# Kernel tuning notes

Hardware: AMD Instinct MI355X
Metric: run time of the kernel (lower is better)

Reference implementation:

```python
import jax, jax.numpy as jnp
import numpy as np

N_NODES = 100000
N_EDGES = 3200000
IN_FEATS = 128
OUT_FEATS = 16
NEG_SLOPE = 0.2


def setup_inputs() -> dict:
    key = jax.random.key(0)
    k1, k2, k3, k4, k5, k6 = jax.random.split(key, 6)
    h = jax.random.normal(k1, (N_NODES, IN_FEATS), dtype=jnp.float32)
    src = jax.random.randint(k2, (N_EDGES,), 0, N_NODES, dtype=jnp.int64)
    dst = jax.random.randint(k3, (N_EDGES,), 0, N_NODES, dtype=jnp.int64)
    W = jax.random.normal(k4, (OUT_FEATS, IN_FEATS), dtype=jnp.float32) * (1.0 / np.sqrt(IN_FEATS))
    a_l = jax.random.normal(k5, (1, OUT_FEATS), dtype=jnp.float32) * (1.0 / np.sqrt(OUT_FEATS))
    a_r = jax.random.normal(k6, (1, OUT_FEATS), dtype=jnp.float32) * (1.0 / np.sqrt(OUT_FEATS))
    return {"h": h, "src": src, "dst": dst, "W": W, "a_l": a_l, "a_r": a_r}


def reference(h, src, dst, W, a_l, a_r):
    N = h.shape[0]
    # node projection: h @ fc.weight.T  -> [N, out]
    hW = h @ W.T
    # per-node attention logits: [N, 1]
    el = hW @ a_l.T
    er = hW @ a_r.T
    # u_add_v: per-edge logit e = el[src] + er[dst], then leaky_relu(0.2)
    e = jax.nn.leaky_relu(el[src] + er[dst], negative_slope=NEG_SLOPE)  # [E, 1]
    # edge_softmax over edges grouped by destination node (numerically stable)
    emax = jax.ops.segment_max(e, dst, num_segments=N)  # [N, 1], -inf for empty
    emax = jnp.where(jnp.isfinite(emax), emax, 0.0)
    e_exp = jnp.exp(e - emax[dst])
    esum = jax.ops.segment_sum(e_exp, dst, num_segments=N)  # [N, 1]
    alpha = e_exp / jnp.maximum(esum[dst], 1e-16)  # [E, 1]
    # u_mul_e + sum: weighted aggregation of source features at destinations
    out = jax.ops.segment_sum(hW[src] * alpha, dst, num_segments=N)  # [N, out]
    return out
```

## Files before the change

### kernel.cpp

```cpp
#include <hip/hip_runtime.h>
#include <hip/hip_bf16.h>
#include <stdint.h>

#define IN_F 128
#define OUT_F 16
#define NEG_SLOPE 0.2f
#define LB_BITS 7
#define LB_NODES 128
#define NB 782
#define CAP 4608
#define SC_E 8192

#define SMEM_BYTES (12512 + 1024 + SC_E * 4)

__device__ __forceinline__ float u2f(uint32_t u) {
  union { uint32_t i; float f; } c;
  c.i = u;
  return c.f;
}

__global__ __launch_bounds__(256) void proj_scatter_kernel(
    const float* __restrict__ h, const float* __restrict__ W,
    const float* __restrict__ a_l, const float* __restrict__ a_r,
    const int* __restrict__ src, const int* __restrict__ dst,
    __hip_bfloat16* __restrict__ hWbf, float* __restrict__ el,
    float* __restrict__ er, int* __restrict__ cursor,
    uint32_t* __restrict__ payload, int N, int E, int scatBlocks) {
  __shared__ __align__(16) uint8_t smem[SMEM_BYTES];
  int t = threadIdx.x;

  if ((int)blockIdx.x < scatBlocks) {
    int* hist = (int*)smem;
    int* pref = hist + NB;
    int* gbase = pref + NB;
    int* rank = gbase + NB;
    int* tsum = rank + NB;
    uint32_t* sortedP = (uint32_t*)(tsum + 256);

    int start = blockIdx.x * SC_E;
    int end = min(E, start + SC_E);
    int cnt = end - start;

    for (int i = t; i < NB; i += 256) { hist[i] = 0; rank[i] = 0; }
    __syncthreads();

    const int4* d4 = (const int4*)(dst + start);
    int n4 = cnt >> 2;
    for (int i = t; i < n4; i += 256) {
      int4 d = d4[i];
      atomicAdd(&hist[d.x >> LB_BITS], 1);
      atomicAdd(&hist[d.y >> LB_BITS], 1);
      atomicAdd(&hist[d.z >> LB_BITS], 1);
      atomicAdd(&hist[d.w >> LB_BITS], 1);
    }
    for (int i = start + (n4 << 2) + t; i < end; i += 256)
      atomicAdd(&hist[dst[i] >> LB_BITS], 1);
    __syncthreads();

    {
      int b0 = t * 4;
      int s_loc = 0;
      if (b0 < NB) {
        int lim = min(b0 + 4, NB);
        for (int j = b0; j < lim; ++j) s_loc += hist[j];
      }
      tsum[t] = s_loc;
    }
    __syncthreads();
    {
      int pre = 0;
      for (int j = 0; j < t; ++j) pre += tsum[j];
      int b0 = t * 4;
      if (b0 < NB) {
        int lim = min(b0 + 4, NB);
        int run = pre;
        for (int j = b0; j < lim; ++j) {
          pref[j] = run;
          int c = hist[j];
          run += c;
          gbase[j] = c ? atomicAdd(&cursor[j * 16], c) : 0;
        }
      }
    }
    __syncthreads();

    const int4* s4 = (const int4*)(src + start);
    for (int i = t; i < n4; i += 256) {
      int4 d = d4[i];
      int4 s = s4[i];
#pragma unroll
      for (int j = 0; j < 4; ++j) {
        int dd = j == 0 ? d.x : j == 1 ? d.y : j == 2 ? d.z : d.w;
        int ss = j == 0 ? s.x : j == 1 ? s.y : j == 2 ? s.z : s.w;
        int b = dd >> LB_BITS;
        int r = atomicAdd(&rank[b], 1);
        sortedP[pref[b] + r] =
            ((uint32_t)ss << LB_BITS) | (uint32_t)(dd & (LB_NODES - 1));
      }
    }
    for (int i = start + (n4 << 2) + t; i < end; i += 256) {
      int dd = dst[i];
      int b = dd >> LB_BITS;
      int r = atomicAdd(&rank[b], 1);
      sortedP[pref[b] + r] =
          ((uint32_t)src[i] << LB_BITS) | (uint32_t)(dd & (LB_NODES - 1));
    }
    __syncthreads();

    int g16 = t >> 4, l16 = t & 15;
    for (int b = g16; b < NB; b += 16) {
      int c = hist[b];
      if (c == 0) continue;
      int p0 = pref[b];
      int gb = gbase[b];
      size_t g0 = (size_t)b * CAP + (size_t)gb;
      for (int j = l16; j < c; j += 16)
        if (gb + j < CAP) payload[g0 + j] = sortedP[p0 + j];
    }
  } else {
    float* Ws = (float*)smem;
    for (int i = t; i < OUT_F * IN_F; i += 256) Ws[i] = W[i];
    __syncthreads();

    int node = ((int)blockIdx.x - scatBlocks) * 256 + t;
    if (node >= N) return;

    const float4* hrow = (const float4*)(h + (size_t)node * IN_F);
    float acc[OUT_F];
#pragma unroll
    for (int f = 0; f < OUT_F; ++f) acc[f] = 0.f;

#pragma unroll 4
    for (int k = 0; k < IN_F / 4; ++k) {
      float4 hv = hrow[k];
#pragma unroll
      for (int f = 0; f < OUT_F; ++f) {
        float4 wv = ((const float4*)(Ws + f * IN_F))[k];
        acc[f] += hv.x * wv.x + hv.y * wv.y + hv.z * wv.z + hv.w * wv.w;
      }
    }

    union {
      unsigned short us[OUT_F];
      uint4 q[2];
    } pk;
#pragma unroll
    for (int f = 0; f < OUT_F; ++f) {
      __hip_bfloat16 b = __float2bfloat16(acc[f]);
      pk.us[f] = *reinterpret_cast<unsigned short*>(&b);
    }
    uint4* dstq = (uint4*)(hWbf + (size_t)node * OUT_F);
    dstq[0] = pk.q[0];
    dstq[1] = pk.q[1];

    float vl = 0.f, vr = 0.f;
#pragma unroll
    for (int f = 0; f < OUT_F; ++f) {
      vl += acc[f] * a_l[f];
      vr += acc[f] * a_r[f];
    }
    el[node] = vl;
    er[node] = vr;
  }
}

__global__ __launch_bounds__(512) void agg_kernel(
    const uint32_t* __restrict__ payload, const int* __restrict__ cursor,
    const __hip_bfloat16* __restrict__ hWbf, const float* __restrict__ el,
    const float* __restrict__ er, float* __restrict__ out, int N) {
  __shared__ __align__(16) uint32_t sorted[CAP];
  __shared__ __align__(16) float exS[CAP];
  __shared__ int hist[LB_NODES];
  __shared__ int pref[LB_NODES];
  __shared__ int rank[LB_NODES];
  uint32_t* kept = (uint32_t*)exS;

  int t = threadIdx.x;
  int b = blockIdx.x;
  size_t base = (size_t)b * CAP;
  int cnt = min(cursor[b * 16], CAP);
  int node0 = b << LB_BITS;

  if (t < LB_NODES) { hist[t] = 0; rank[t] = 0; }
  __syncthreads();

  const uint4* pay4 = (const uint4*)(payload + base);
  uint4* kept4 = (uint4*)kept;
  int n4 = (cnt + 3) >> 2;
  for (int i = t; i < n4; i += 512) {
    uint4 v = pay4[i];
    kept4[i] = v;
    int i0 = i << 2;
    if (i0 + 0 < cnt) atomicAdd(&hist[v.x & (LB_NODES - 1)], 1);
    if (i0 + 1 < cnt) atomicAdd(&hist[v.y & (LB_NODES - 1)], 1);
    if (i0 + 2 < cnt) atomicAdd(&hist[v.z & (LB_NODES - 1)], 1);
    if (i0 + 3 < cnt) atomicAdd(&hist[v.w & (LB_NODES - 1)], 1);
  }
  __syncthreads();

  if (t < LB_NODES) {
    int s = 0;
    for (int j = 0; j < t; ++j) s += hist[j];
    pref[t] = s;
  }
  __syncthreads();

  for (int i = t; i < cnt; i += 512) {
    uint32_t p = kept[i];
    int dl = (int)(p & (LB_NODES - 1));
    int r = atomicAdd(&rank[dl], 1);
    sorted[pref[dl] + r] = p;
  }
  __syncthreads();

  for (int i = t; i < cnt; i += 512) {
    uint32_t p = sorted[i];
    float x = el[p >> LB_BITS] + er[node0 + (int)(p & (LB_NODES - 1))];
    x = x > 0.f ? x : NEG_SLOPE * x;
    exS[i] = __expf(x);
  }
  __syncthreads();

  int g = t >> 2, f4 = t & 3;
  int node = node0 + g;
  if (node < N) {
    int k = pref[g];
    int kend = k + hist[g];
    float a0 = 0.f, a1 = 0.f, a2 = 0.f, a3 = 0.f, es = 0.f;
    const uint2* hw2 = (const uint2*)hWbf;
#pragma unroll 4
    for (; k < kend; ++k) {
      uint32_t p = sorted[k];
      float ex = exS[k];
      uint2 w = hw2[(size_t)(p >> LB_BITS) * 4 + f4];
      a0 += ex * u2f(w.x << 16);
      a1 += ex * u2f(w.x & 0xffff0000u);
      a2 += ex * u2f(w.y << 16);
      a3 += ex * u2f(w.y & 0xffff0000u);
      es += ex;
    }
    float inv = 1.0f / fmaxf(es, 1e-16f);
    float4 o = make_float4(a0 * inv, a1 * inv, a2 * inv, a3 * inv);
    ((float4*)(out + (size_t)node * OUT_F))[f4] = o;
  }
}

extern "C" void kernel_launch(void* const* d_in, const int* in_sizes, int n_in,
                              void* d_out, int out_size, void* d_ws, size_t ws_size,
                              hipStream_t stream) {
  const float* h   = (const float*)d_in[0];
  const int*   src = (const int*)d_in[1];
  const int*   dst = (const int*)d_in[2];
  const float* W   = (const float*)d_in[3];
  const float* a_l = (const float*)d_in[4];
  const float* a_r = (const float*)d_in[5];
  float* out = (float*)d_out;

  const int N = in_sizes[0] / IN_F;
  const int E = in_sizes[1];
  const int scatBlocks = (E + SC_E - 1) / SC_E;
  const int projBlocks = (N + 255) / 256;

  __hip_bfloat16* hWbf = (__hip_bfloat16*)d_ws;
  float* el = (float*)(hWbf + (size_t)N * OUT_F);
  float* er = el + N;
  int* cursor = (int*)(er + N);
  uint32_t* payload = (uint32_t*)(cursor + (size_t)NB * 16);

  hipMemsetAsync(cursor, 0, (size_t)NB * 16 * sizeof(int), stream);

  proj_scatter_kernel<<<scatBlocks + projBlocks, 256, 0, stream>>>(
      h, W, a_l, a_r, src, dst, hWbf, el, er, cursor, payload, N, E, scatBlocks);

  agg_kernel<<<NB, 512, 0, stream>>>(payload, cursor, hWbf, el, er, out, N);
}
```

Before: 180.9 us.

## Widen proj/scatter blocks, two nodes per projection thread, fuse agg exp pass

The fused projection/scatter kernel now runs 512-thread blocks. The scatter path reuses the histogram as the rank counter and derives bucket counts from a prefix array with a sentinel entry, which saves shared memory. Each projection thread computes two node rows so every shared W load serves two rows. In the aggregation kernel the payload staging copy is removed: the counting-sort pass rereads payload from global memory, computes the exponentiated logit inline using er values cached in shared memory, and drops one pass and one barrier. The risks are higher register pressure from the dual accumulators and a second global read of the payload.

```diff
diff --git a/kernel.cpp b/kernel.cpp
--- a/kernel.cpp
+++ b/kernel.cpp
@@ -10,8 +10,9 @@
 #define NB 782
 #define CAP 4608
 #define SC_E 8192
-
-#define SMEM_BYTES (12512 + 1024 + SC_E * 4)
+#define PROJ_M 2
+
+#define SMEM_BYTES (11436 + SC_E * 4)
 
 __device__ __forceinline__ float u2f(uint32_t u) {
   union { uint32_t i; float f; } c;
@@ -19,7 +20,7 @@
   return c.f;
 }
 
-__global__ __launch_bounds__(256) void proj_scatter_kernel(
+__global__ __launch_bounds__(512, 6) void proj_scatter_kernel(
     const float* __restrict__ h, const float* __restrict__ W,
     const float* __restrict__ a_l, const float* __restrict__ a_r,
     const int* __restrict__ src, const int* __restrict__ dst,
@@ -32,36 +33,35 @@
   if ((int)blockIdx.x < scatBlocks) {
     int* hist = (int*)smem;
     int* pref = hist + NB;
-    int* gbase = pref + NB;
-    int* rank = gbase + NB;
-    int* tsum = rank + NB;
-    uint32_t* sortedP = (uint32_t*)(tsum + 256);
+    int* gbase = pref + NB + 1;
+    int* tsum = gbase + NB;
+    uint32_t* sortedP = (uint32_t*)(tsum + 512);
 
     int start = blockIdx.x * SC_E;
     int end = min(E, start + SC_E);
     int cnt = end - start;
 
-    for (int i = t; i < NB; i += 256) { hist[i] = 0; rank[i] = 0; }
+    for (int i = t; i < NB; i += 512) hist[i] = 0;
     __syncthreads();
 
     const int4* d4 = (const int4*)(dst + start);
     int n4 = cnt >> 2;
-    for (int i = t; i < n4; i += 256) {
+    for (int i = t; i < n4; i += 512) {
       int4 d = d4[i];
       atomicAdd(&hist[d.x >> LB_BITS], 1);
       atomicAdd(&hist[d.y >> LB_BITS], 1);
       atomicAdd(&hist[d.z >> LB_BITS], 1);
       atomicAdd(&hist[d.w >> LB_BITS], 1);
     }
-    for (int i = start + (n4 << 2) + t; i < end; i += 256)
+    for (int i = start + (n4 << 2) + t; i < end; i += 512)
       atomicAdd(&hist[dst[i] >> LB_BITS], 1);
     __syncthreads();
 
     {
-      int b0 = t * 4;
+      int b0 = t * 2;
       int s_loc = 0;
       if (b0 < NB) {
-        int lim = min(b0 + 4, NB);
+        int lim = min(b0 + 2, NB);
         for (int j = b0; j < lim; ++j) s_loc += hist[j];
       }
       tsum[t] = s_loc;
@@ -70,22 +70,24 @@
     {
       int pre = 0;
       for (int j = 0; j < t; ++j) pre += tsum[j];
-      int b0 = t * 4;
+      int b0 = t * 2;
       if (b0 < NB) {
-        int lim = min(b0 + 4, NB);
+        int lim = min(b0 + 2, NB);
         int run = pre;
         for (int j = b0; j < lim; ++j) {
           pref[j] = run;
           int c = hist[j];
           run += c;
           gbase[j] = c ? atomicAdd(&cursor[j * 16], c) : 0;
+          hist[j] = 0;
         }
+        if (lim == NB) pref[NB] = run;
       }
     }
     __syncthreads();
 
     const int4* s4 = (const int4*)(src + start);
-    for (int i = t; i < n4; i += 256) {
+    for (int i = t; i < n4; i += 512) {
       int4 d = d4[i];
       int4 s = s4[i];
 #pragma unroll
@@ -93,25 +95,25 @@
         int dd = j == 0 ? d.x : j == 1 ? d.y : j == 2 ? d.z : d.w;
         int ss = j == 0 ? s.x : j == 1 ? s.y : j == 2 ? s.z : s.w;
         int b = dd >> LB_BITS;
-        int r = atomicAdd(&rank[b], 1);
+        int r = atomicAdd(&hist[b], 1);
         sortedP[pref[b] + r] =
             ((uint32_t)ss << LB_BITS) | (uint32_t)(dd & (LB_NODES - 1));
       }
     }
-    for (int i = start + (n4 << 2) + t; i < end; i += 256) {
+    for (int i = start + (n4 << 2) + t; i < end; i += 512) {
       int dd = dst[i];
       int b = dd >> LB_BITS;
-      int r = atomicAdd(&rank[b], 1);
+      int r = atomicAdd(&hist[b], 1);
       sortedP[pref[b] + r] =
           ((uint32_t)src[i] << LB_BITS) | (uint32_t)(dd & (LB_NODES - 1));
     }
     __syncthreads();
 
     int g16 = t >> 4, l16 = t & 15;
-    for (int b = g16; b < NB; b += 16) {
-      int c = hist[b];
+    for (int b = g16; b < NB; b += 32) {
+      int p0 = pref[b];
+      int c = pref[b + 1] - p0;
       if (c == 0) continue;
-      int p0 = pref[b];
       int gb = gbase[b];
       size_t g0 = (size_t)b * CAP + (size_t)gb;
       for (int j = l16; j < c; j += 16)
@@ -119,24 +121,30 @@
     }
   } else {
     float* Ws = (float*)smem;
-    for (int i = t; i < OUT_F * IN_F; i += 256) Ws[i] = W[i];
-    __syncthreads();
-
-    int node = ((int)blockIdx.x - scatBlocks) * 256 + t;
-    if (node >= N) return;
-
-    const float4* hrow = (const float4*)(h + (size_t)node * IN_F);
-    float acc[OUT_F];
-#pragma unroll
-    for (int f = 0; f < OUT_F; ++f) acc[f] = 0.f;
-
-#pragma unroll 4
+    for (int i = t; i < OUT_F * IN_F; i += 512) Ws[i] = W[i];
+    __syncthreads();
+
+    int blk = (int)blockIdx.x - scatBlocks;
+    int n0 = blk * (512 * PROJ_M) + t;
+    int n1 = n0 + 512;
+    bool v1 = n1 < N;
+    if (n0 >= N) return;
+
+    const float4* r0 = (const float4*)(h + (size_t)n0 * IN_F);
+    const float4* r1 = (const float4*)(h + (size_t)(v1 ? n1 : n0) * IN_F);
+
+    float acc0[OUT_F], acc1[OUT_F];
+#pragma unroll
+    for (int f = 0; f < OUT_F; ++f) { acc0[f] = 0.f; acc1[f] = 0.f; }
+
     for (int k = 0; k < IN_F / 4; ++k) {
-      float4 hv = hrow[k];
+      float4 h0 = r0[k];
+      float4 h1 = r1[k];
 #pragma unroll
       for (int f = 0; f < OUT_F; ++f) {
         float4 wv = ((const float4*)(Ws + f * IN_F))[k];
-        acc[f] += hv.x * wv.x + hv.y * wv.y + hv.z * wv.z + hv.w * wv.w;
+        acc0[f] += h0.x * wv.x + h0.y * wv.y + h0.z * wv.z + h0.w * wv.w;
+        acc1[f] += h1.x * wv.x + h1.y * wv.y + h1.z * wv.z + h1.w * wv.w;
       }
     }
 
@@ -146,21 +154,40 @@
     } pk;
 #pragma unroll
     for (int f = 0; f < OUT_F; ++f) {
-      __hip_bfloat16 b = __float2bfloat16(acc[f]);
+      __hip_bfloat16 b = __float2bfloat16(acc0[f]);
       pk.us[f] = *reinterpret_cast<unsigned short*>(&b);
     }
-    uint4* dstq = (uint4*)(hWbf + (size_t)node * OUT_F);
-    dstq[0] = pk.q[0];
-    dstq[1] = pk.q[1];
+    uint4* dq0 = (uint4*)(hWbf + (size_t)n0 * OUT_F);
+    dq0[0] = pk.q[0];
+    dq0[1] = pk.q[1];
 
     float vl = 0.f, vr = 0.f;
 #pragma unroll
     for (int f = 0; f < OUT_F; ++f) {
-      vl += acc[f] * a_l[f];
-      vr += acc[f] * a_r[f];
-    }
-    el[node] = vl;
-    er[node] = vr;
+      vl += acc0[f] * a_l[f];
+      vr += acc0[f] * a_r[f];
+    }
+    el[n0] = vl;
+    er[n0] = vr;
+
+    if (v1) {
+#pragma unroll
+      for (int f = 0; f < OUT_F; ++f) {
+        __hip_bfloat16 b = __float2bfloat16(acc1[f]);
+        pk.us[f] = *reinterpret_cast<unsigned short*>(&b);
+      }
+      uint4* dq1 = (uint4*)(hWbf + (size_t)n1 * OUT_F);
+      dq1[0] = pk.q[0];
+      dq1[1] = pk.q[1];
+      float wl = 0.f, wr = 0.f;
+#pragma unroll
+      for (int f = 0; f < OUT_F; ++f) {
+        wl += acc1[f] * a_l[f];
+        wr += acc1[f] * a_r[f];
+      }
+      el[n1] = wl;
+      er[n1] = wr;
+    }
   }
 }
 
@@ -173,7 +200,7 @@
   __shared__ int hist[LB_NODES];
   __shared__ int pref[LB_NODES];
   __shared__ int rank[LB_NODES];
-  uint32_t* kept = (uint32_t*)exS;
+  __shared__ float erS[LB_NODES];
 
   int t = threadIdx.x;
   int b = blockIdx.x;
@@ -181,15 +208,18 @@
   int cnt = min(cursor[b * 16], CAP);
   int node0 = b << LB_BITS;
 
-  if (t < LB_NODES) { hist[t] = 0; rank[t] = 0; }
+  if (t < LB_NODES) {
+    hist[t] = 0;
+    rank[t] = 0;
+    int nd = node0 + t;
+    erS[t] = nd < N ? er[nd] : 0.f;
+  }
   __syncthreads();
 
   const uint4* pay4 = (const uint4*)(payload + base);
-  uint4* kept4 = (uint4*)kept;
   int n4 = (cnt + 3) >> 2;
   for (int i = t; i < n4; i += 512) {
     uint4 v = pay4[i];
-    kept4[i] = v;
     int i0 = i << 2;
     if (i0 + 0 < cnt) atomicAdd(&hist[v.x & (LB_NODES - 1)], 1);
     if (i0 + 1 < cnt) atomicAdd(&hist[v.y & (LB_NODES - 1)], 1);
@@ -206,18 +236,14 @@
   __syncthreads();
 
   for (int i = t; i < cnt; i += 512) {
-    uint32_t p = kept[i];
+    uint32_t p = payload[base + i];
     int dl = (int)(p & (LB_NODES - 1));
     int r = atomicAdd(&rank[dl], 1);
-    sorted[pref[dl] + r] = p;
-  }
-  __syncthreads();
-
-  for (int i = t; i < cnt; i += 512) {
-    uint32_t p = sorted[i];
-    float x = el[p >> LB_BITS] + er[node0 + (int)(p & (LB_NODES - 1))];
+    int pos = pref[dl] + r;
+    sorted[pos] = p;
+    float x = el[p >> LB_BITS] + erS[dl];
     x = x > 0.f ? x : NEG_SLOPE * x;
-    exS[i] = __expf(x);
+    exS[pos] = __expf(x);
   }
   __syncthreads();
 
@@ -259,7 +285,7 @@
   const int N = in_sizes[0] / IN_F;
   const int E = in_sizes[1];
   const int scatBlocks = (E + SC_E - 1) / SC_E;
-  const int projBlocks = (N + 255) / 256;
+  const int projBlocks = (N + 512 * PROJ_M - 1) / (512 * PROJ_M);
 
   __hip_bfloat16* hWbf = (__hip_bfloat16*)d_ws;
   float* el = (float*)(hWbf + (size_t)N * OUT_F);
@@ -269,7 +295,7 @@
 
   hipMemsetAsync(cursor, 0, (size_t)NB * 16 * sizeof(int), stream);
 
-  proj_scatter_kernel<<<scatBlocks + projBlocks, 256, 0, stream>>>(
+  proj_scatter_kernel<<<scatBlocks + projBlocks, 512, 0, stream>>>(
       h, W, a_l, a_r, src, dst, hWbf, el, er, cursor, payload, N, E, scatBlocks);
 
   agg_kernel<<<NB, 512, 0, stream>>>(payload, cursor, hWbf, el, er, out, N);
```

Result: slower. 195.0 us (+7.8%).

## Fuse memset, scatter/projection and aggregation into one cooperative kernel

Applied to the files above, without the earlier changes.

Replaces the memset plus two kernel launches with a single cooperative kernel that zeroes the cursors, runs scatter and projection, then aggregation, separated by grid-wide syncs. The aim is to remove launch gaps and tail effects between stages. It also shrinks shared memory with 16-bit prefix arrays, switches to a wave-shuffle scan, fuses the sort and exp passes in aggregation, caches er in shared memory, and uses 256 threads with 8 features per thread. Grid sync only works if all ~1175 blocks fit co-resident; the cooperative launch may fail, in which case it falls back to separate launches.

```diff
diff --git a/kernel.cpp b/kernel.cpp
--- a/kernel.cpp
+++ b/kernel.cpp
@@ -1,6 +1,9 @@
 #include <hip/hip_runtime.h>
 #include <hip/hip_bf16.h>
+#include <hip/hip_cooperative_groups.h>
 #include <stdint.h>
+
+namespace cg = cooperative_groups;
 
 #define IN_F 128
 #define OUT_F 16
@@ -11,7 +14,20 @@
 #define CAP 4608
 #define SC_E 8192
 
-#define SMEM_BYTES (12512 + 1024 + SC_E * 4)
+#define OFF_HIST 0
+#define OFF_WSUM 3136
+#define OFF_PREF 3152
+#define OFF_GBASE 4720
+#define OFF_SORTP 6400
+#define SMEM_FUSED 39168
+
+#define AOFF_SORTED 0
+#define AOFF_EXS 18432
+#define AOFF_HIST 36864
+#define AOFF_PREF 37376
+#define AOFF_RANK 37888
+#define AOFF_ERS 38400
+#define SMEM_AGG 38912
 
 __device__ __forceinline__ float u2f(uint32_t u) {
   union { uint32_t i; float f; } c;
@@ -19,247 +35,329 @@
   return c.f;
 }
 
-__global__ __launch_bounds__(256) void proj_scatter_kernel(
+__device__ __forceinline__ void scatter_phase(
+    uint8_t* smem, const int* __restrict__ src, const int* __restrict__ dst,
+    int* cursor, uint32_t* payload, int E, int sbid) {
+  int t = threadIdx.x;
+  int lane = t & 63, wv = t >> 6;
+  int* hist = (int*)(smem + OFF_HIST);
+  int* wsum = (int*)(smem + OFF_WSUM);
+  unsigned short* pref = (unsigned short*)(smem + OFF_PREF);
+  unsigned short* gbase = (unsigned short*)(smem + OFF_GBASE);
+  uint32_t* sortedP = (uint32_t*)(smem + OFF_SORTP);
+
+  int start = sbid * SC_E;
+  int end = min(E, start + SC_E);
+  int cnt = end - start;
+
+  for (int i = t; i < NB; i += 256) hist[i] = 0;
+  __syncthreads();
+
+  const int4* d4 = (const int4*)(dst + start);
+  int n4 = cnt >> 2;
+  for (int i = t; i < n4; i += 256) {
+    int4 d = d4[i];
+    atomicAdd(&hist[d.x >> LB_BITS], 1);
+    atomicAdd(&hist[d.y >> LB_BITS], 1);
+    atomicAdd(&hist[d.z >> LB_BITS], 1);
+    atomicAdd(&hist[d.w >> LB_BITS], 1);
+  }
+  for (int i = start + (n4 << 2) + t; i < end; i += 256)
+    atomicAdd(&hist[dst[i] >> LB_BITS], 1);
+  __syncthreads();
+
+  int b0 = t * 4;
+  int c0 = (b0 < NB) ? hist[b0] : 0;
+  int c1 = (b0 + 1 < NB) ? hist[b0 + 1] : 0;
+  int c2 = (b0 + 2 < NB) ? hist[b0 + 2] : 0;
+  int c3 = (b0 + 3 < NB) ? hist[b0 + 3] : 0;
+  int s_loc = c0 + c1 + c2 + c3;
+  int inc = s_loc;
+#pragma unroll
+  for (int off = 1; off < 64; off <<= 1) {
+    int v = __shfl_up(inc, off, 64);
+    if (lane >= off) inc += v;
+  }
+  if (lane == 63) wsum[wv] = inc;
+  __syncthreads();
+  int run = inc - s_loc;
+#pragma unroll
+  for (int w = 0; w < 4; ++w)
+    if (w < wv) run += wsum[w];
+  if (b0 < NB) {
+    pref[b0] = (unsigned short)run;
+    int g = c0 ? atomicAdd(&cursor[b0 * 16], c0) : 0;
+    gbase[b0] = (unsigned short)min(g, 65535);
+    hist[b0] = 0;
+    run += c0;
+    if (b0 == NB - 1) pref[NB] = (unsigned short)run;
+  }
+  if (b0 + 1 < NB) {
+    pref[b0 + 1] = (unsigned short)run;
+    int g = c1 ? atomicAdd(&cursor[(b0 + 1) * 16], c1) : 0;
+    gbase[b0 + 1] = (unsigned short)min(g, 65535);
+    hist[b0 + 1] = 0;
+    run += c1;
+    if (b0 + 1 == NB - 1) pref[NB] = (unsigned short)run;
+  }
+  if (b0 + 2 < NB) {
+    pref[b0 + 2] = (unsigned short)run;
+    int g = c2 ? atomicAdd(&cursor[(b0 + 2) * 16], c2) : 0;
+    gbase[b0 + 2] = (unsigned short)min(g, 65535);
+    hist[b0 + 2] = 0;
+    run += c2;
+    if (b0 + 2 == NB - 1) pref[NB] = (unsigned short)run;
+  }
+  if (b0 + 3 < NB) {
+    pref[b0 + 3] = (unsigned short)run;
+    int g = c3 ? atomicAdd(&cursor[(b0 + 3) * 16], c3) : 0;
+    gbase[b0 + 3] = (unsigned short)min(g, 65535);
+    hist[b0 + 3] = 0;
+    run += c3;
+    if (b0 + 3 == NB - 1) pref[NB] = (unsigned short)run;
+  }
+  __syncthreads();
+
+  const int4* s4 = (const int4*)(src + start);
+  for (int i = t; i < n4; i += 256) {
+    int4 d = d4[i];
+    int4 s = s4[i];
+#pragma unroll
+    for (int j = 0; j < 4; ++j) {
+      int dd = j == 0 ? d.x : j == 1 ? d.y : j == 2 ? d.z : d.w;
+      int ss = j == 0 ? s.x : j == 1 ? s.y : j == 2 ? s.z : s.w;
+      int b = dd >> LB_BITS;
+      int r = atomicAdd(&hist[b], 1);
+      sortedP[(int)pref[b] + r] =
+          ((uint32_t)ss << LB_BITS) | (uint32_t)(dd & (LB_NODES - 1));
+    }
+  }
+  for (int i = start + (n4 << 2) + t; i < end; i += 256) {
+    int dd = dst[i];
+    int b = dd >> LB_BITS;
+    int r = atomicAdd(&hist[b], 1);
+    sortedP[(int)pref[b] + r] =
+        ((uint32_t)src[i] << LB_BITS) | (uint32_t)(dd & (LB_NODES - 1));
+  }
+  __syncthreads();
+
+  int g16 = t >> 4, l16 = t & 15;
+  for (int b = g16; b < NB; b += 16) {
+    int p0 = pref[b];
+    int c = (int)pref[b + 1] - p0;
+    if (c == 0) continue;
+    int gb = gbase[b];
+    size_t g0 = (size_t)b * CAP + (size_t)gb;
+    for (int j = l16; j < c; j += 16)
+      if (gb + j < CAP) payload[g0 + j] = sortedP[p0 + j];
+  }
+}
+
+__device__ __forceinline__ void proj_phase(
+    uint8_t* smem, const float* __restrict__ h, const float* __restrict__ W,
+    const float* __restrict__ a_l, const float* __restrict__ a_r,
+    __hip_bfloat16* __restrict__ hWbf, float* __restrict__ el,
+    float* __restrict__ er, int N, int pbid) {
+  float* Ws = (float*)smem;
+  int t = threadIdx.x;
+  for (int i = t; i < OUT_F * IN_F; i += 256) Ws[i] = W[i];
+  __syncthreads();
+
+  int node = pbid * 256 + t;
+  if (node < N) {
+    const float4* hrow = (const float4*)(h + (size_t)node * IN_F);
+    float acc[OUT_F];
+#pragma unroll
+    for (int f = 0; f < OUT_F; ++f) acc[f] = 0.f;
+
+#pragma unroll 4
+    for (int k = 0; k < IN_F / 4; ++k) {
+      float4 hv = hrow[k];
+#pragma unroll
+      for (int f = 0; f < OUT_F; ++f) {
+        float4 wv = ((const float4*)(Ws + f * IN_F))[k];
+        acc[f] += hv.x * wv.x + hv.y * wv.y + hv.z * wv.z + hv.w * wv.w;
+      }
+    }
+
+    union {
+      unsigned short us[OUT_F];
+      uint4 q[2];
+    } pk;
+#pragma unroll
+    for (int f = 0; f < OUT_F; ++f) {
+      __hip_bfloat16 b = __float2bfloat16(acc[f]);
+      pk.us[f] = *reinterpret_cast<unsigned short*>(&b);
+    }
+    uint4* dstq = (uint4*)(hWbf + (size_t)node * OUT_F);
+    dstq[0] = pk.q[0];
+    dstq[1] = pk.q[1];
+
+    float vl = 0.f, vr = 0.f;
+#pragma unroll
+    for (int f = 0; f < OUT_F; ++f) {
+      vl += acc[f] * a_l[f];
+      vr += acc[f] * a_r[f];
+    }
+    el[node] = vl;
+    er[node] = vr;
+  }
+}
+
+__device__ __forceinline__ void agg_phase(
+    uint8_t* smem, const uint32_t* __restrict__ payload,
+    const int* __restrict__ cursor, const __hip_bfloat16* __restrict__ hWbf,
+    const float* __restrict__ el, const float* __restrict__ er,
+    float* __restrict__ out, int N, int b) {
+  uint32_t* sorted = (uint32_t*)(smem + AOFF_SORTED);
+  float* exS = (float*)(smem + AOFF_EXS);
+  int* hist = (int*)(smem + AOFF_HIST);
+  int* pref = (int*)(smem + AOFF_PREF);
+  int* rank = (int*)(smem + AOFF_RANK);
+  float* erS = (float*)(smem + AOFF_ERS);
+
+  int t = threadIdx.x;
+  size_t base = (size_t)b * CAP;
+  int cnt = min(cursor[b * 16], CAP);
+  int node0 = b << LB_BITS;
+
+  if (t < LB_NODES) {
+    hist[t] = 0;
+    rank[t] = 0;
+    int nd = node0 + t;
+    erS[t] = nd < N ? er[nd] : 0.f;
+  }
+  __syncthreads();
+
+  const uint4* pay4 = (const uint4*)(payload + base);
+  int n4 = (cnt + 3) >> 2;
+  for (int i = t; i < n4; i += 256) {
+    uint4 v = pay4[i];
+    int i0 = i << 2;
+    if (i0 + 0 < cnt) atomicAdd(&hist[v.x & (LB_NODES - 1)], 1);
+    if (i0 + 1 < cnt) atomicAdd(&hist[v.y & (LB_NODES - 1)], 1);
+    if (i0 + 2 < cnt) atomicAdd(&hist[v.z & (LB_NODES - 1)], 1);
+    if (i0 + 3 < cnt) atomicAdd(&hist[v.w & (LB_NODES - 1)], 1);
+  }
+  __syncthreads();
+
+  if (t < LB_NODES) {
+    int s = 0;
+    for (int j = 0; j < t; ++j) s += hist[j];
+    pref[t] = s;
+  }
+  __syncthreads();
+
+  for (int i = t; i < cnt; i += 256) {
+    uint32_t p = payload[base + i];
+    int dl = (int)(p & (LB_NODES - 1));
+    int r = atomicAdd(&rank[dl], 1);
+    int pos = pref[dl] + r;
+    sorted[pos] = p;
+    float x = el[p >> LB_BITS] + erS[dl];
+    x = x > 0.f ? x : NEG_SLOPE * x;
+    exS[pos] = __expf(x);
+  }
+  __syncthreads();
+
+  int g = t >> 1, f8 = t & 1;
+  int node = node0 + g;
+  if (node < N) {
+    int k = pref[g];
+    int kend = k + hist[g];
+    float a0 = 0, a1 = 0, a2 = 0, a3 = 0, a4 = 0, a5 = 0, a6 = 0, a7 = 0,
+          es = 0;
+    const uint4* hw4 = (const uint4*)hWbf;
+#pragma unroll 4
+    for (; k < kend; ++k) {
+      uint32_t p = sorted[k];
+      float ex = exS[k];
+      uint4 w = hw4[(size_t)(p >> LB_BITS) * 2 + f8];
+      a0 += ex * u2f(w.x << 16);
+      a1 += ex * u2f(w.x & 0xffff0000u);
+      a2 += ex * u2f(w.y << 16);
+      a3 += ex * u2f(w.y & 0xffff0000u);
+      a4 += ex * u2f(w.z << 16);
+      a5 += ex * u2f(w.z & 0xffff0000u);
+      a6 += ex * u2f(w.w << 16);
+      a7 += ex * u2f(w.w & 0xffff0000u);
+      es += ex;
+    }
+    float inv = 1.0f / fmaxf(es, 1e-16f);
+    float4* op = (float4*)(out + (size_t)node * OUT_F + f8 * 8);
+    op[0] = make_float4(a0 * inv, a1 * inv, a2 * inv, a3 * inv);
+    op[1] = make_float4(a4 * inv, a5 * inv, a6 * inv, a7 * inv);
+  }
+  __syncthreads();
+}
+
+__global__ __launch_bounds__(256, 4) void gat_fused(
+    const float* __restrict__ h, const float* __restrict__ W,
+    const float* __restrict__ a_l, const float* __restrict__ a_r,
+    const int* __restrict__ src, const int* __restrict__ dst,
+    __hip_bfloat16* __restrict__ hWbf, float* __restrict__ el,
+    float* __restrict__ er, int* __restrict__ cursor,
+    uint32_t* __restrict__ payload, float* __restrict__ out, int N, int E,
+    int scatBlocks) {
+  __shared__ __align__(16) uint8_t smem[SMEM_FUSED];
+  int bid = blockIdx.x, t = threadIdx.x;
+  cg::grid_group grid = cg::this_grid();
+
+  for (int i = bid * 256 + t; i < NB * 16; i += (int)gridDim.x * 256)
+    cursor[i] = 0;
+  __threadfence();
+  grid.sync();
+
+  if (bid < scatBlocks)
+    scatter_phase(smem, src, dst, cursor, payload, E, bid);
+  else
+    proj_phase(smem, h, W, a_l, a_r, hWbf, el, er, N, bid - scatBlocks);
+  __threadfence();
+  grid.sync();
+
+  if (bid < NB)
+    agg_phase(smem, payload, cursor, hWbf, el, er, out, N, bid);
+}
+
+__global__ __launch_bounds__(256) void ps_kernel(
     const float* __restrict__ h, const float* __restrict__ W,
     const float* __restrict__ a_l, const float* __restrict__ a_r,
     const int* __restrict__ src, const int* __restrict__ dst,
     __hip_bfloat16* __restrict__ hWbf, float* __restrict__ el,
     float* __restrict__ er, int* __restrict__ cursor,
     uint32_t* __restrict__ payload, int N, int E, int scatBlocks) {
-  __shared__ __align__(16) uint8_t smem[SMEM_BYTES];
-  int t = threadIdx.x;
-
-  if ((int)blockIdx.x < scatBlocks) {
-    int* hist = (int*)smem;
-    int* pref = hist + NB;
-    int* gbase = pref + NB;
-    int* rank = gbase + NB;
-    int* tsum = rank + NB;
-    uint32_t* sortedP = (uint32_t*)(tsum + 256);
-
-    int start = blockIdx.x * SC_E;
-    int end = min(E, start + SC_E);
-    int cnt = end - start;
-
-    for (int i = t; i < NB; i += 256) { hist[i] = 0; rank[i] = 0; }
-    __syncthreads();
-
-    const int4* d4 = (const int4*)(dst + start);
-    int n4 = cnt >> 2;
-    for (int i = t; i < n4; i += 256) {
-      int4 d = d4[i];
-      atomicAdd(&hist[d.x >> LB_BITS], 1);
-      atomicAdd(&hist[d.y >> LB_BITS], 1);
-      atomicAdd(&hist[d.z >> LB_BITS], 1);
-      atomicAdd(&hist[d.w >> LB_BITS], 1);
-    }
-    for (int i = start + (n4 << 2) + t; i < end; i += 256)
-      atomicAdd(&hist[dst[i] >> LB_BITS], 1);
-    __syncthreads();
-
-    {
-      int b0 = t * 4;
-      int s_loc = 0;
-      if (b0 < NB) {
-        int lim = min(b0 + 4, NB);
-        for (int j = b0; j < lim; ++j) s_loc += hist[j];
-      }
-      tsum[t] = s_loc;
-    }
-    __syncthreads();
-    {
-      int pre = 0;
-      for (int j = 0; j < t; ++j) pre += tsum[j];
-      int b0 = t * 4;
-      if (b0 < NB) {
-        int lim = min(b0 + 4, NB);
-        int run = pre;
-        for (int j = b0; j < lim; ++j) {
-          pref[j] = run;
-          int c = hist[j];
-          run += c;
-          gbase[j] = c ? atomicAdd(&cursor[j * 16], c) : 0;
-        }
-      }
-    }
-    __syncthreads();
-
-    const int4* s4 = (const int4*)(src + start);
-    for (int i = t; i < n4; i += 256) {
-      int4 d = d4[i];
-      int4 s = s4[i];
-#pragma unroll
-      for (int j = 0; j < 4; ++j) {
-        int dd = j == 0 ? d.x : j == 1 ? d.y : j == 2 ? d.z : d.w;
-        int ss = j == 0 ? s.x : j == 1 ? s.y : j == 2 ? s.z : s.w;
-        int b = dd >> LB_BITS;
-        int r = atomicAdd(&rank[b], 1);
-        sortedP[pref[b] + r] =
-            ((uint32_t)ss << LB_BITS) | (uint32_t)(dd & (LB_NODES - 1));
-      }
-    }
-    for (int i = start + (n4 << 2) + t; i < end; i += 256) {
-      int dd = dst[i];
-      int b = dd >> LB_BITS;
-      int r = atomicAdd(&rank[b], 1);
-      sortedP[pref[b] + r] =
-          ((uint32_t)src[i] << LB_BITS) | (uint32_t)(dd & (LB_NODES - 1));
-    }
-    __syncthreads();
-
-    int g16 = t >> 4, l16 = t & 15;
-    for (int b = g16; b < NB; b += 16) {
-      int c = hist[b];
-      if (c == 0) continue;
-      int p0 = pref[b];
-      int gb = gbase[b];
-      size_t g0 = (size_t)b * CAP + (size_t)gb;
-      for (int j = l16; j < c; j += 16)
-        if (gb + j < CAP) payload[g0 + j] = sortedP[p0 + j];
-    }
-  } else {
-    float* Ws = (float*)smem;
-    for (int i = t; i < OUT_F * IN_F; i += 256) Ws[i] = W[i];
-    __syncthreads();
-
-    int node = ((int)blockIdx.x - scatBlocks) * 256 + t;
-    if (node >= N) return;
-
-    const float4* hrow = (const float4*)(h + (size_t)node * IN_F);
-    float acc[OUT_F];
-#pragma unroll
-    for (int f = 0; f < OUT_F; ++f) acc[f] = 0.f;
-
-#pragma unroll 4
-    for (int k = 0; k < IN_F / 4; ++k) {
-      float4 hv = hrow[k];
-#pragma unroll
-      for (int f = 0; f < OUT_F; ++f) {
-        float4 wv = ((const float4*)(Ws + f * IN_F))[k];
-        acc[f] += hv.x * wv.x + hv.y * wv.y + hv.z * wv.z + hv.w * wv.w;
-      }
-    }
-
-    union {
-      unsigned short us[OUT_F];
-      uint4 q[2];
-    } pk;
-#pragma unroll
-    for (int f = 0; f < OUT_F; ++f) {
-      __hip_bfloat16 b = __float2bfloat16(acc[f]);
-      pk.us[f] = *reinterpret_cast<unsigned short*>(&b);
-    }
-    uint4* dstq = (uint4*)(hWbf + (size_t)node * OUT_F);
-    dstq[0] = pk.q[0];
-    dstq[1] = pk.q[1];
-
-    float vl = 0.f, vr = 0.f;
-#pragma unroll
-    for (int f = 0; f < OUT_F; ++f) {
-      vl += acc[f] * a_l[f];
-      vr += acc[f] * a_r[f];
-    }
-    el[node] = vl;
-    er[node] = vr;
-  }
-}
-
-__global__ __launch_bounds__(512) void agg_kernel(
+  __shared__ __align__(16) uint8_t smem[SMEM_FUSED];
+  if ((int)blockIdx.x < scatBlocks)
+    scatter_phase(smem, src, dst, cursor, payload, E, blockIdx.x);
+  else
+    proj_phase(smem, h, W, a_l, a_r, hWbf, el, er, N,
+               (int)blockIdx.x - scatBlocks);
+}
+
+__global__ __launch_bounds__(256) void agg_kernel(
     const uint32_t* __restrict__ payload, const int* __restrict__ cursor,
     const __hip_bfloat16* __restrict__ hWbf, const float* __restrict__ el,
     const float* __restrict__ er, float* __restrict__ out, int N) {
-  __shared__ __align__(16) uint32_t sorted[CAP];
-  __shared__ __align__(16) float exS[CAP];
-  __shared__ int hist[LB_NODES];
-  __shared__ int pref[LB_NODES];
-  __shared__ int rank[LB_NODES];
-  uint32_t* kept = (uint32_t*)exS;
-
-  int t = threadIdx.x;
-  int b = blockIdx.x;
-  size_t base = (size_t)b * CAP;
-  int cnt = min(cursor[b * 16], CAP);
-  int node0 = b << LB_BITS;
-
-  if (t < LB_NODES) { hist[t] = 0; rank[t] = 0; }
-  __syncthreads();
-
-  const uint4* pay4 = (const uint4*)(payload + base);
-  uint4* kept4 = (uint4*)kept;
-  int n4 = (cnt + 3) >> 2;
-  for (int i = t; i < n4; i += 512) {
-    uint4 v = pay4[i];
-    kept4[i] = v;
-    int i0 = i << 2;
-    if (i0 + 0 < cnt) atomicAdd(&hist[v.x & (LB_NODES - 1)], 1);
-    if (i0 + 1 < cnt) atomicAdd(&hist[v.y & (LB_NODES - 1)], 1);
-    if (i0 + 2 < cnt) atomicAdd(&hist[v.z & (LB_NODES - 1)], 1);
-    if (i0 + 3 < cnt) atomicAdd(&hist[v.w & (LB_NODES - 1)], 1);
-  }
-  __syncthreads();
-
-  if (t < LB_NODES) {
-    int s = 0;
-    for (int j = 0; j < t; ++j) s += hist[j];
-    pref[t] = s;
-  }
-  __syncthreads();
-
-  for (int i = t; i < cnt; i += 512) {
-    uint32_t p = kept[i];
-    int dl = (int)(p & (LB_NODES - 1));
-    int r = atomicAdd(&rank[dl], 1);
-    sorted[pref[dl] + r] = p;
-  }
-  __syncthreads();
-
-  for (int i = t; i < cnt; i += 512) {
-    uint32_t p = sorted[i];
-    float x = el[p >> LB_BITS] + er[node0 + (int)(p & (LB_NODES - 1))];
-    x = x > 0.f ? x : NEG_SLOPE * x;
-    exS[i] = __expf(x);
-  }
-  __syncthreads();
-
-  int g = t >> 2, f4 = t & 3;
-  int node = node0 + g;
-  if (node < N) {
-    int k = pref[g];
-    int kend = k + hist[g];
-    float a0 = 0.f, a1 = 0.f, a2 = 0.f, a3 = 0.f, es = 0.f;
-    const uint2* hw2 = (const uint2*)hWbf;
-#pragma unroll 4
-    for (; k < kend; ++k) {
-      uint32_t p = sorted[k];
-      float ex = exS[k];
-      uint2 w = hw2[(size_t)(p >> LB_BITS) * 4 + f4];
-      a0 += ex * u2f(w.x << 16);
-      a1 += ex * u2f(w.x & 0xffff0000u);
-      a2 += ex * u2f(w.y << 16);
-      a3 += ex * u2f(w.y & 0xffff0000u);
-      es += ex;
-    }
-    float inv = 1.0f / fmaxf(es, 1e-16f);
-    float4 o = make_float4(a0 * inv, a1 * inv, a2 * inv, a3 * inv);
-    ((float4*)(out + (size_t)node * OUT_F))[f4] = o;
-  }
+  __shared__ __align__(16) uint8_t smem[SMEM_AGG];
+  agg_phase(smem, payload, cursor, hWbf, el, er, out, N, blockIdx.x);
 }
 
 extern "C" void kernel_launch(void* const* d_in, const int* in_sizes, int n_in,
-                              void* d_out, int out_size, void* d_ws, size_t ws_size,
-                              hipStream_t stream) {
-  const float* h   = (const float*)d_in[0];
-  const int*   src = (const int*)d_in[1];
-  const int*   dst = (const int*)d_in[2];
-  const float* W   = (const float*)d_in[3];
+                              void* d_out, int out_size, void* d_ws,
+                              size_t ws_size, hipStream_t stream) {
+  const float* h = (const float*)d_in[0];
+  const int* src = (const int*)d_in[1];
+  const int* dst = (const int*)d_in[2];
+  const float* W = (const float*)d_in[3];
   const float* a_l = (const float*)d_in[4];
   const float* a_r = (const float*)d_in[5];
   float* out = (float*)d_out;
 
-  const int N = in_sizes[0] / IN_F;
-  const int E = in_sizes[1];
-  const int scatBlocks = (E + SC_E - 1) / SC_E;
-  const int projBlocks = (N + 255) / 256;
+  int N = in_sizes[0] / IN_F;
+  int E = in_sizes[1];
+  int scatBlocks = (E + SC_E - 1) / SC_E;
+  int projBlocks = (N + 255) / 256;
+  int grid = scatBlocks + projBlocks;
 
   __hip_bfloat16* hWbf = (__hip_bfloat16*)d_ws;
   float* el = (float*)(hWbf + (size_t)N * OUT_F);
@@ -267,10 +365,16 @@
   int* cursor = (int*)(er + N);
   uint32_t* payload = (uint32_t*)(cursor + (size_t)NB * 16);
 
-  hipMemsetAsync(cursor, 0, (size_t)NB * 16 * sizeof(int), stream);
-
-  proj_scatter_kernel<<<scatBlocks + projBlocks, 256, 0, stream>>>(
-      h, W, a_l, a_r, src, dst, hWbf, el, er, cursor, payload, N, E, scatBlocks);
-
-  agg_kernel<<<NB, 512, 0, stream>>>(payload, cursor, hWbf, el, er, out, N);
-}
+  void* args[] = {&h,  &W,  &a_l,    &a_r,     &src, &dst, &hWbf, &el,
+                  &er, &cursor, &payload, &out, &N,   &E,   &scatBlocks};
+  hipError_t err = hipLaunchCooperativeKernel((const void*)gat_fused,
+                                              dim3(grid), dim3(256), args, 0,
+                                              stream);
+  if (err != hipSuccess) {
+    (void)hipGetLastError();
+    hipMemsetAsync(cursor, 0, (size_t)NB * 16 * sizeof(int), stream);
+    ps_kernel<<<grid, 256, 0, stream>>>(h, W, a_l, a_r, src, dst, hWbf, el, er,
+                                        cursor, payload, N, E, scatBlocks);
+    agg_kernel<<<NB, 256, 0, stream>>>(payload, cursor, hWbf, el, er, out, N);
+  }
+}
```

Result: slower. 447.2 us (+147.2%).

## Replace block-local bucket sort with per-edge global atomics into sub-bucketed payload

Applied to the files above, without the earlier changes.

The scatter phase drops the shared-memory histogram/prefix/sort per 8192-edge chunk and instead has each edge atomically claim a slot in one of 16 sub-buckets per 128-node bucket, directly in global memory. The aggregation kernel reads the 16 sub-buckets, caches er in shared memory, and fuses the local sort with the exp computation into packed (payload, exp) pairs. The aim is to remove several block syncs and the staging copy, at the cost of about 3.2M global atomics with contention spread over 16 cursor copies, and scattered 4-byte global writes. Per-sub-bucket capacity of 384 can silently drop edges if a bucket's load is skewed.

```diff
diff --git a/kernel.cpp b/kernel.cpp
--- a/kernel.cpp
+++ b/kernel.cpp
@@ -8,10 +8,10 @@
 #define LB_BITS 7
 #define LB_NODES 128
 #define NB 782
-#define CAP 4608
-#define SC_E 8192
-
-#define SMEM_BYTES (12512 + 1024 + SC_E * 4)
+#define NSUB 16
+#define SUBCAP 384
+#define CAP (NSUB * SUBCAP)
+#define LCAP 4608
 
 __device__ __forceinline__ float u2f(uint32_t u) {
   union { uint32_t i; float f; } c;
@@ -26,99 +26,41 @@
     __hip_bfloat16* __restrict__ hWbf, float* __restrict__ el,
     float* __restrict__ er, int* __restrict__ cursor,
     uint32_t* __restrict__ payload, int N, int E, int scatBlocks) {
-  __shared__ __align__(16) uint8_t smem[SMEM_BYTES];
+  __shared__ __align__(16) float Ws[OUT_F * IN_F];
   int t = threadIdx.x;
 
   if ((int)blockIdx.x < scatBlocks) {
-    int* hist = (int*)smem;
-    int* pref = hist + NB;
-    int* gbase = pref + NB;
-    int* rank = gbase + NB;
-    int* tsum = rank + NB;
-    uint32_t* sortedP = (uint32_t*)(tsum + 256);
-
-    int start = blockIdx.x * SC_E;
-    int end = min(E, start + SC_E);
-    int cnt = end - start;
-
-    for (int i = t; i < NB; i += 256) { hist[i] = 0; rank[i] = 0; }
-    __syncthreads();
-
-    const int4* d4 = (const int4*)(dst + start);
-    int n4 = cnt >> 2;
-    for (int i = t; i < n4; i += 256) {
+    int wid = (int)blockIdx.x * 4 + (t >> 6);
+    int s = wid & (NSUB - 1);
+    int* curS = cursor + s * NB;
+
+    const int4* d4 = (const int4*)dst;
+    const int4* s4 = (const int4*)src;
+    int n4 = E >> 2;
+    int stride = scatBlocks * 256;
+    for (int i = (int)blockIdx.x * 256 + t; i < n4; i += stride) {
       int4 d = d4[i];
-      atomicAdd(&hist[d.x >> LB_BITS], 1);
-      atomicAdd(&hist[d.y >> LB_BITS], 1);
-      atomicAdd(&hist[d.z >> LB_BITS], 1);
-      atomicAdd(&hist[d.w >> LB_BITS], 1);
-    }
-    for (int i = start + (n4 << 2) + t; i < end; i += 256)
-      atomicAdd(&hist[dst[i] >> LB_BITS], 1);
-    __syncthreads();
-
-    {
-      int b0 = t * 4;
-      int s_loc = 0;
-      if (b0 < NB) {
-        int lim = min(b0 + 4, NB);
-        for (int j = b0; j < lim; ++j) s_loc += hist[j];
-      }
-      tsum[t] = s_loc;
-    }
-    __syncthreads();
-    {
-      int pre = 0;
-      for (int j = 0; j < t; ++j) pre += tsum[j];
-      int b0 = t * 4;
-      if (b0 < NB) {
-        int lim = min(b0 + 4, NB);
-        int run = pre;
-        for (int j = b0; j < lim; ++j) {
-          pref[j] = run;
-          int c = hist[j];
-          run += c;
-          gbase[j] = c ? atomicAdd(&cursor[j * 16], c) : 0;
-        }
-      }
-    }
-    __syncthreads();
-
-    const int4* s4 = (const int4*)(src + start);
-    for (int i = t; i < n4; i += 256) {
-      int4 d = d4[i];
-      int4 s = s4[i];
+      int4 sv = s4[i];
 #pragma unroll
       for (int j = 0; j < 4; ++j) {
         int dd = j == 0 ? d.x : j == 1 ? d.y : j == 2 ? d.z : d.w;
-        int ss = j == 0 ? s.x : j == 1 ? s.y : j == 2 ? s.z : s.w;
+        int ss = j == 0 ? sv.x : j == 1 ? sv.y : j == 2 ? sv.z : sv.w;
         int b = dd >> LB_BITS;
-        int r = atomicAdd(&rank[b], 1);
-        sortedP[pref[b] + r] =
-            ((uint32_t)ss << LB_BITS) | (uint32_t)(dd & (LB_NODES - 1));
+        int r = atomicAdd(&curS[b], 1);
+        if (r < SUBCAP)
+          payload[(size_t)b * CAP + s * SUBCAP + r] =
+              ((uint32_t)ss << LB_BITS) | (uint32_t)(dd & (LB_NODES - 1));
       }
     }
-    for (int i = start + (n4 << 2) + t; i < end; i += 256) {
+    for (int i = (n4 << 2) + (int)blockIdx.x * 256 + t; i < E; i += stride) {
       int dd = dst[i];
       int b = dd >> LB_BITS;
-      int r = atomicAdd(&rank[b], 1);
-      sortedP[pref[b] + r] =
-          ((uint32_t)src[i] << LB_BITS) | (uint32_t)(dd & (LB_NODES - 1));
-    }
-    __syncthreads();
-
-    int g16 = t >> 4, l16 = t & 15;
-    for (int b = g16; b < NB; b += 16) {
-      int c = hist[b];
-      if (c == 0) continue;
-      int p0 = pref[b];
-      int gb = gbase[b];
-      size_t g0 = (size_t)b * CAP + (size_t)gb;
-      for (int j = l16; j < c; j += 16)
-        if (gb + j < CAP) payload[g0 + j] = sortedP[p0 + j];
+      int r = atomicAdd(&curS[b], 1);
+      if (r < SUBCAP)
+        payload[(size_t)b * CAP + s * SUBCAP + r] =
+            ((uint32_t)src[i] << LB_BITS) | (uint32_t)(dd & (LB_NODES - 1));
     }
   } else {
-    float* Ws = (float*)smem;
     for (int i = t; i < OUT_F * IN_F; i += 256) Ws[i] = W[i];
     __syncthreads();
 
@@ -168,33 +110,32 @@
     const uint32_t* __restrict__ payload, const int* __restrict__ cursor,
     const __hip_bfloat16* __restrict__ hWbf, const float* __restrict__ el,
     const float* __restrict__ er, float* __restrict__ out, int N) {
-  __shared__ __align__(16) uint32_t sorted[CAP];
-  __shared__ __align__(16) float exS[CAP];
+  __shared__ __align__(16) uint2 pairs[LCAP];
   __shared__ int hist[LB_NODES];
   __shared__ int pref[LB_NODES];
   __shared__ int rank[LB_NODES];
-  uint32_t* kept = (uint32_t*)exS;
+  __shared__ float erS[LB_NODES];
+  __shared__ int cntS[NSUB];
 
   int t = threadIdx.x;
   int b = blockIdx.x;
   size_t base = (size_t)b * CAP;
-  int cnt = min(cursor[b * 16], CAP);
   int node0 = b << LB_BITS;
 
-  if (t < LB_NODES) { hist[t] = 0; rank[t] = 0; }
-  __syncthreads();
-
-  const uint4* pay4 = (const uint4*)(payload + base);
-  uint4* kept4 = (uint4*)kept;
-  int n4 = (cnt + 3) >> 2;
-  for (int i = t; i < n4; i += 512) {
-    uint4 v = pay4[i];
-    kept4[i] = v;
-    int i0 = i << 2;
-    if (i0 + 0 < cnt) atomicAdd(&hist[v.x & (LB_NODES - 1)], 1);
-    if (i0 + 1 < cnt) atomicAdd(&hist[v.y & (LB_NODES - 1)], 1);
-    if (i0 + 2 < cnt) atomicAdd(&hist[v.z & (LB_NODES - 1)], 1);
-    if (i0 + 3 < cnt) atomicAdd(&hist[v.w & (LB_NODES - 1)], 1);
+  if (t < LB_NODES) {
+    hist[t] = 0;
+    rank[t] = 0;
+    int nd = node0 + t;
+    erS[t] = nd < N ? er[nd] : 0.f;
+  }
+  if (t < NSUB) cntS[t] = min(cursor[t * NB + b], SUBCAP);
+  __syncthreads();
+
+  for (int s = 0; s < NSUB; ++s) {
+    int cs = cntS[s];
+    const uint32_t* sub = payload + base + s * SUBCAP;
+    for (int i = t; i < cs; i += 512)
+      atomicAdd(&hist[sub[i] & (LB_NODES - 1)], 1);
   }
   __syncthreads();
 
@@ -205,19 +146,18 @@
   }
   __syncthreads();
 
-  for (int i = t; i < cnt; i += 512) {
-    uint32_t p = kept[i];
-    int dl = (int)(p & (LB_NODES - 1));
-    int r = atomicAdd(&rank[dl], 1);
-    sorted[pref[dl] + r] = p;
-  }
-  __syncthreads();
-
-  for (int i = t; i < cnt; i += 512) {
-    uint32_t p = sorted[i];
-    float x = el[p >> LB_BITS] + er[node0 + (int)(p & (LB_NODES - 1))];
-    x = x > 0.f ? x : NEG_SLOPE * x;
-    exS[i] = __expf(x);
+  for (int s = 0; s < NSUB; ++s) {
+    int cs = cntS[s];
+    const uint32_t* sub = payload + base + s * SUBCAP;
+    for (int i = t; i < cs; i += 512) {
+      uint32_t p = sub[i];
+      int dl = (int)(p & (LB_NODES - 1));
+      int r = atomicAdd(&rank[dl], 1);
+      int pos = pref[dl] + r;
+      float x = el[p >> LB_BITS] + erS[dl];
+      x = x > 0.f ? x : NEG_SLOPE * x;
+      if (pos < LCAP) pairs[pos] = make_uint2(p, __float_as_uint(__expf(x)));
+    }
   }
   __syncthreads();
 
@@ -225,14 +165,14 @@
   int node = node0 + g;
   if (node < N) {
     int k = pref[g];
-    int kend = k + hist[g];
+    int kend = min(k + hist[g], LCAP);
     float a0 = 0.f, a1 = 0.f, a2 = 0.f, a3 = 0.f, es = 0.f;
     const uint2* hw2 = (const uint2*)hWbf;
 #pragma unroll 4
     for (; k < kend; ++k) {
-      uint32_t p = sorted[k];
-      float ex = exS[k];
-      uint2 w = hw2[(size_t)(p >> LB_BITS) * 4 + f4];
+      uint2 q = pairs[k];
+      float ex = __uint_as_float(q.y);
+      uint2 w = hw2[(size_t)(q.x >> LB_BITS) * 4 + f4];
       a0 += ex * u2f(w.x << 16);
       a1 += ex * u2f(w.x & 0xffff0000u);
       a2 += ex * u2f(w.y << 16);
@@ -258,16 +198,16 @@
 
   const int N = in_sizes[0] / IN_F;
   const int E = in_sizes[1];
-  const int scatBlocks = (E + SC_E - 1) / SC_E;
+  const int scatBlocks = 782;
   const int projBlocks = (N + 255) / 256;
 
   __hip_bfloat16* hWbf = (__hip_bfloat16*)d_ws;
   float* el = (float*)(hWbf + (size_t)N * OUT_F);
   float* er = el + N;
   int* cursor = (int*)(er + N);
-  uint32_t* payload = (uint32_t*)(cursor + (size_t)NB * 16);
-
-  hipMemsetAsync(cursor, 0, (size_t)NB * 16 * sizeof(int), stream);
+  uint32_t* payload = (uint32_t*)(cursor + (size_t)NSUB * NB);
+
+  hipMemsetAsync(cursor, 0, (size_t)NSUB * NB * sizeof(int), stream);
 
   proj_scatter_kernel<<<scatBlocks + projBlocks, 256, 0, stream>>>(
       h, W, a_l, a_r, src, dst, hWbf, el, er, cursor, payload, N, E, scatBlocks);
```

Measured after the change: 251.8 us. 1.39x slower.
